# Performance work log

Hardware: AMD Instinct MI355X
Metric: run time of the kernel (lower is better)

## Reference

```python
import jax, jax.numpy as jnp
import numpy as np

EPS = 1e-5

def _ln(x, g, b):
    m = x.mean(-1, keepdims=True)
    v = ((x - m) ** 2).mean(-1, keepdims=True)
    return (x - m) * jax.lax.rsqrt(v + EPS) * g + b

def _tshift(x):
    # ZeroPad2d((0,0,1,-1)): xx[:, t] = x[:, t-1], xx[:, 0] = 0
    return jnp.concatenate([jnp.zeros_like(x[:, :1]), x[:, :-1]], axis=1)

def _wkv(time_decay, time_first, k, v):
    # Numerically-stable RWKV-4 WKV recurrence. k, v: (B, T, D)
    w = -jnp.exp(time_decay)  # (D,) negative decay
    u = time_first
    kT = jnp.swapaxes(k, 0, 1)  # (T, B, D)
    vT = jnp.swapaxes(v, 0, 1)
    a0 = jnp.zeros(kT.shape[1:], k.dtype)
    init = (a0, a0, jnp.full_like(a0, -1e30))  # a, b, p (running max exponent)
    def step(carry, kv_t):
        a, b, p = carry
        kt, vt = kv_t
        ww = u + kt
        q = jnp.maximum(p, ww)
        e1 = jnp.exp(p - q)
        e2 = jnp.exp(ww - q)
        y = (e1 * a + e2 * vt) / (e1 * b + e2)
        ww2 = p + w
        q2 = jnp.maximum(ww2, kt)
        e1b = jnp.exp(ww2 - q2)
        e2b = jnp.exp(kt - q2)
        return (e1b * a + e2b * vt, e1b * b + e2b, q2), y
    _, y = jax.lax.scan(step, init, (kT, vT))
    return jnp.swapaxes(y, 0, 1)

def setup_inputs() -> dict:
    key = jax.random.key(0)
    B, T, C, DA, DF = 8, 2048, 1024, 1024, 4096
    n_layer, layer_id = 12, 1
    ks = jax.random.split(key, 10)
    s = 0.02
    # faithful RWKV time-mixing inits
    r01 = layer_id / (n_layer - 1)
    r1a0 = 1.0 - layer_id / n_layer
    ddd = (np.arange(C) / C).astype(np.float32)
    decay_speed = (-5 + 8 * (np.arange(DA) / (DA - 1)) ** (0.7 + 1.3 * r01)).astype(np.float32)
    zigzag = (np.array([(i + 1) % 3 - 1 for i in range(DA)], dtype=np.float32)) * 0.5
    inp = {
        'x': jax.random.normal(ks[0], (B, T, C), jnp.float32),
        'ln1_g': jnp.ones((C,)), 'ln1_b': jnp.zeros((C,)),
        'ln2_g': jnp.ones((C,)), 'ln2_b': jnp.zeros((C,)),
        'tm_k': jnp.asarray(ddd ** r1a0),
        'tm_v': jnp.asarray(ddd ** r1a0 + 0.3 * r01),
        'tm_r': jnp.asarray(ddd ** (0.5 * r1a0)),
        'time_decay': jnp.asarray(decay_speed),
        'time_first': jnp.asarray(np.float32(np.log(0.3)) + zigzag),
        'Wk': jax.random.normal(ks[1], (DA, C), jnp.float32) * s,
        'Wv': jax.random.normal(ks[2], (DA, C), jnp.float32) * s,
        'Wr': jax.random.normal(ks[3], (DA, C), jnp.float32) * s,
        'Wo': jax.random.normal(ks[4], (C, DA), jnp.float32) * s,
        'fm_k': jnp.asarray(ddd ** r1a0),
        'fm_r': jnp.asarray(ddd ** r1a0),
        'Fk': jax.random.normal(ks[5], (DF, C), jnp.float32) * s,
        'Fr': jax.random.normal(ks[6], (C, C), jnp.float32) * s,
        'Fv': jax.random.normal(ks[7], (C, DF), jnp.float32) * s,
    }
    return inp

def reference(x, ln1_g, ln1_b, ln2_g, ln2_b, tm_k, tm_v, tm_r, time_decay, time_first,
              Wk, Wv, Wr, Wo, fm_k, fm_r, Fk, Fr, Fv):
    # --- TimeMix (RWKV attention) ---
    h = _ln(x, ln1_g, ln1_b)
    hh = _tshift(h)
    xk = h * tm_k + hh * (1 - tm_k)
    xv = h * tm_v + hh * (1 - tm_v)
    xr = h * tm_r + hh * (1 - tm_r)
    k = jnp.einsum('btc,dc->btd', xk, Wk)
    v = jnp.einsum('btc,dc->btd', xv, Wv)
    sr = jax.nn.sigmoid(jnp.einsum('btc,dc->btd', xr, Wr))
    rwkv = sr * _wkv(time_decay, time_first, k, v)
    x = x + jnp.einsum('btd,cd->btc', rwkv, Wo)
    # --- ChannelMix ---
    g = _ln(x, ln2_g, ln2_b)
    gg = _tshift(g)
    gk = g * fm_k + gg * (1 - fm_k)
    gr = g * fm_r + gg * (1 - fm_r)
    kf = jnp.square(jax.nn.relu(jnp.einsum('btc,fc->btf', gk, Fk)))
    kv = jnp.einsum('btf,cf->btc', kf, Fv)
    x = x + jax.nn.sigmoid(jnp.einsum('btc,dc->btd', gr, Fr)) * kv
    return x
```

## Files before the change

kernel.cpp:

```cpp
#include <hip/hip_runtime.h>
#include <stdint.h>

typedef __attribute__((ext_vector_type(4))) float f32x4;
typedef __attribute__((ext_vector_type(8))) __bf16 bfv8;

__device__ __forceinline__ ushort f2bf(float f) {
  union { float f; uint32_t u; } c; c.f = f;
  uint32_t u = c.u;
  uint32_t r = (u + 0x7fffu + ((u >> 16) & 1u)) >> 16;
  return (ushort)r;
}
__device__ __forceinline__ float bf2f(ushort h) {
  union { uint32_t u; float f; } c;
  c.u = ((uint32_t)h) << 16;
  return c.f;
}

__global__ void cvt_bf16(const float* __restrict__ src, ushort* __restrict__ dst, int n4) {
  int i = blockIdx.x * blockDim.x + threadIdx.x;
  if (i < n4) {
    float4 f = ((const float4*)src)[i];
    ushort4 o;
    o.x = f2bf(f.x); o.y = f2bf(f.y); o.z = f2bf(f.z); o.w = f2bf(f.w);
    ((ushort4*)dst)[i] = o;
  }
}

template <int NOUT, bool BI>
__global__ __launch_bounds__(256)
void ln_mix(const void* __restrict__ xin, const float* __restrict__ gam,
            const float* __restrict__ bet, const float* __restrict__ mk,
            const float* __restrict__ mv, const float* __restrict__ mr,
            ushort* __restrict__ ok, ushort* __restrict__ ov,
            ushort* __restrict__ orr, int T, int C) {
  const int row = blockIdx.x;
  const int t = row % T;
  const int tid = threadIdx.x;
  float4 c4, p4 = make_float4(0.f, 0.f, 0.f, 0.f);
  if constexpr (BI) {
    const ushort4* xc = (const ushort4*)((const ushort*)xin + (size_t)row * C);
    ushort4 u = xc[tid];
    c4 = make_float4(bf2f(u.x), bf2f(u.y), bf2f(u.z), bf2f(u.w));
    if (t > 0) {
      ushort4 up = xc[tid - (C >> 2)];
      p4 = make_float4(bf2f(up.x), bf2f(up.y), bf2f(up.z), bf2f(up.w));
    }
  } else {
    const float4* xc = (const float4*)((const float*)xin + (size_t)row * C);
    c4 = xc[tid];
    if (t > 0) p4 = xc[tid - (C >> 2)];
  }

  float s = c4.x + c4.y + c4.z + c4.w;
  float ss = c4.x * c4.x + c4.y * c4.y + c4.z * c4.z + c4.w * c4.w;
  float s2 = p4.x + p4.y + p4.z + p4.w;
  float ss2 = p4.x * p4.x + p4.y * p4.y + p4.z * p4.z + p4.w * p4.w;
#pragma unroll
  for (int off = 32; off > 0; off >>= 1) {
    s += __shfl_down(s, off);
    ss += __shfl_down(ss, off);
    s2 += __shfl_down(s2, off);
    ss2 += __shfl_down(ss2, off);
  }
  __shared__ float red[4][4];
  const int wid = tid >> 6, lane = tid & 63;
  if (lane == 0) { red[wid][0] = s; red[wid][1] = ss; red[wid][2] = s2; red[wid][3] = ss2; }
  __syncthreads();
  s = red[0][0] + red[1][0] + red[2][0] + red[3][0];
  ss = red[0][1] + red[1][1] + red[2][1] + red[3][1];
  s2 = red[0][2] + red[1][2] + red[2][2] + red[3][2];
  ss2 = red[0][3] + red[1][3] + red[2][3] + red[3][3];

  const float invC = 1.0f / (float)C;
  float m1 = s * invC, v1 = ss * invC - m1 * m1;
  float rs1 = rsqrtf(v1 + 1e-5f);
  float m2 = s2 * invC, v2 = ss2 * invC - m2 * m2;
  float rs2 = rsqrtf(v2 + 1e-5f);

  const float* c4p = (const float*)&c4;
  const float* p4p = (const float*)&p4;
  ushort4 vk, vv, vr;
#pragma unroll
  for (int j = 0; j < 4; j++) {
    int col = tid * 4 + j;
    float gg = gam[col], be = bet[col];
    float hc = (c4p[j] - m1) * rs1 * gg + be;
    float hp = (t > 0) ? ((p4p[j] - m2) * rs2 * gg + be) : 0.0f;
    float fk = mk[col];
    ((ushort*)&vk)[j] = f2bf(hc * fk + hp * (1.0f - fk));
    if constexpr (NOUT == 3) {
      float fv = mv[col];
      ((ushort*)&vv)[j] = f2bf(hc * fv + hp * (1.0f - fv));
    }
    float fr = mr[col];
    ((ushort*)&vr)[j] = f2bf(hc * fr + hp * (1.0f - fr));
  }
  size_t o = (size_t)row * (C >> 2) + tid;
  ((ushort4*)ok)[o] = vk;
  if constexpr (NOUT == 3) ((ushort4*)ov)[o] = vv;
  ((ushort4*)orr)[o] = vr;
}

template <int MODE>
__global__ __launch_bounds__(256, 2)
void gemm_bt(const ushort* __restrict__ A, const ushort* __restrict__ W,
             void* __restrict__ outp, const void* __restrict__ res,
             const ushort* __restrict__ mul, int N, int K) {
  __shared__ ushort lA[2][4096];
  __shared__ ushort lB[2][4096];
  const int tid = threadIdx.x;
  const int wave = tid >> 6, lane = tid & 63;

  const int nwg = gridDim.x * gridDim.y;
  const int bid = blockIdx.y * gridDim.x + blockIdx.x;
  const int swz = (bid & 7) * (nwg >> 3) + (bid >> 3);
  const int rowBase = (swz / gridDim.x) * 128;
  const int colBase = (swz % gridDim.x) * 128;

  const int wr = wave >> 1, wc = wave & 1;
  const int lr = lane & 15, lk = lane >> 4;

  f32x4 acc[4][4];
#pragma unroll
  for (int m = 0; m < 4; m++)
#pragma unroll
    for (int n = 0; n < 4; n++) acc[m][n] = (f32x4){0.f, 0.f, 0.f, 0.f};

  const int c0 = wave * 128 + lane;
  const int r0 = c0 >> 2, q0 = (c0 & 3) * 8;
  const int c1 = c0 + 64;
  const int r1 = c1 >> 2, q1 = (c1 & 3) * 8;

  auto stage = [&](int buf, int kt) {
    const ushort* gA0 = A + (size_t)(rowBase + r0) * K + kt + q0;
    const ushort* gA1 = A + (size_t)(rowBase + r1) * K + kt + q1;
    const ushort* gB0 = W + (size_t)(colBase + r0) * K + kt + q0;
    const ushort* gB1 = W + (size_t)(colBase + r1) * K + kt + q1;
    ushort* dA = &lA[buf][wave * 1024];
    ushort* dB = &lB[buf][wave * 1024];
    __builtin_amdgcn_global_load_lds(
        (const __attribute__((address_space(1))) void*)gA0,
        (__attribute__((address_space(3))) void*)dA, 16, 0, 0);
    __builtin_amdgcn_global_load_lds(
        (const __attribute__((address_space(1))) void*)gA1,
        (__attribute__((address_space(3))) void*)(dA + 512), 16, 0, 0);
    __builtin_amdgcn_global_load_lds(
        (const __attribute__((address_space(1))) void*)gB0,
        (__attribute__((address_space(3))) void*)dB, 16, 0, 0);
    __builtin_amdgcn_global_load_lds(
        (const __attribute__((address_space(1))) void*)gB1,
        (__attribute__((address_space(3))) void*)(dB + 512), 16, 0, 0);
  };

  auto compute = [&](int buf) {
    bfv8 af[4], bfr[4];
#pragma unroll
    for (int m = 0; m < 4; m++)
      af[m] = *(const bfv8*)(&lA[buf][(wr * 64 + m * 16 + lr) * 32 + lk * 8]);
#pragma unroll
    for (int n = 0; n < 4; n++)
      bfr[n] = *(const bfv8*)(&lB[buf][(wc * 64 + n * 16 + lr) * 32 + lk * 8]);
#pragma unroll
    for (int m = 0; m < 4; m++)
#pragma unroll
      for (int n = 0; n < 4; n++)
        acc[m][n] = __builtin_amdgcn_mfma_f32_16x16x32_bf16(af[m], bfr[n], acc[m][n], 0, 0, 0);
  };

  stage(0, 0);
  __syncthreads();
  int cur = 0;
  for (int kt = 0; kt + 32 < K; kt += 32) {
    stage(cur ^ 1, kt + 32);
    compute(cur);
    __syncthreads();
    cur ^= 1;
  }
  compute(cur);

#pragma unroll
  for (int m = 0; m < 4; m++) {
#pragma unroll
    for (int j = 0; j < 4; j++) {
      int row = rowBase + wr * 64 + m * 16 + lk * 4 + j;
#pragma unroll
      for (int n = 0; n < 4; n++) {
        int col = colBase + wc * 64 + n * 16 + lr;
        float v = acc[m][n][j];
        size_t idx = (size_t)row * N + col;
        if constexpr (MODE == 0) {
          ((ushort*)outp)[idx] = f2bf(v);
        } else if constexpr (MODE == 1) {
          ((ushort*)outp)[idx] = f2bf(1.0f / (1.0f + __expf(-v)));
        } else if constexpr (MODE == 2) {
          float r = fmaxf(v, 0.0f);
          ((ushort*)outp)[idx] = f2bf(r * r);
        } else if constexpr (MODE == 4) {
          ((float*)outp)[idx] = bf2f(((const ushort*)res)[idx]) + bf2f(mul[idx]) * v;
        } else {
          ((ushort*)outp)[idx] = f2bf(((const float*)res)[idx] + v);
        }
      }
    }
  }
}

#define WKV_NCH 32
#define WKV_L 64

__global__ __launch_bounds__(256)
void wkv_phase1(const ushort* __restrict__ k, const ushort* __restrict__ v,
                const float* __restrict__ td,
                float* __restrict__ sA, float* __restrict__ sB, float* __restrict__ sP,
                int T, int D) {
  int id = blockIdx.x * 256 + threadIdx.x;
  int d = id % D;
  int bc = id / D;
  int c = bc % WKV_NCH;
  int b = bc / WKV_NCH;
  float w = -__expf(td[d]);
  float a = 0.f, bb = 0.f, p = -1e30f;
  const size_t base = (size_t)b * T * D + (size_t)c * WKV_L * D + d;
#pragma unroll 4
  for (int t = 0; t < WKV_L; t++) {
    size_t idx = base + (size_t)t * D;
    float kt = bf2f(k[idx]), vt = bf2f(v[idx]);
    float ww2 = p + w;
    float q2 = fmaxf(ww2, kt);
    float e1b = __expf(ww2 - q2), e2b = __expf(kt - q2);
    a = e1b * a + e2b * vt;
    bb = e1b * bb + e2b;
    p = q2;
  }
  sA[id] = a; sB[id] = bb; sP[id] = p;
}

__global__ __launch_bounds__(256)
void wkv_combine(const float* __restrict__ td,
                 float* __restrict__ sA, float* __restrict__ sB, float* __restrict__ sP,
                 int D) {
  int id = blockIdx.x * 256 + threadIdx.x;
  int d = id % D;
  int b = id / D;
  float w = -__expf(td[d]);
  float Lw = (float)WKV_L * w;
  float a = 0.f, bb = 0.f, p = -1e30f;
  for (int c = 0; c < WKV_NCH; c++) {
    size_t idx = ((size_t)b * WKV_NCH + c) * D + d;
    float la = sA[idx], lb = sB[idx], lp = sP[idx];
    sA[idx] = a; sB[idx] = bb; sP[idx] = p;
    float pd = p + Lw;
    float q = fmaxf(pd, lp);
    float e1 = __expf(pd - q), e2 = __expf(lp - q);
    a = e1 * a + e2 * la;
    bb = e1 * bb + e2 * lb;
    p = q;
  }
}

__global__ __launch_bounds__(256)
void wkv_phase3(const ushort* __restrict__ k, const ushort* __restrict__ v,
                const ushort* __restrict__ sr, const float* __restrict__ td,
                const float* __restrict__ tf,
                const float* __restrict__ sA, const float* __restrict__ sB,
                const float* __restrict__ sP, ushort* __restrict__ out,
                int T, int D) {
  int id = blockIdx.x * 256 + threadIdx.x;
  int d = id % D;
  int bc = id / D;
  int c = bc % WKV_NCH;
  int b = bc / WKV_NCH;
  float w = -__expf(td[d]);
  float u = tf[d];
  float a = sA[id], bb = sB[id], p = sP[id];
  const size_t base = (size_t)b * T * D + (size_t)c * WKV_L * D + d;
#pragma unroll 2
  for (int t = 0; t < WKV_L; t++) {
    size_t idx = base + (size_t)t * D;
    float kt = bf2f(k[idx]), vt = bf2f(v[idx]);
    float ww = u + kt;
    float q = fmaxf(p, ww);
    float e1 = __expf(p - q), e2 = __expf(ww - q);
    float y = (e1 * a + e2 * vt) / (e1 * bb + e2);
    out[idx] = f2bf(bf2f(sr[idx]) * y);
    float ww2 = p + w;
    float q2 = fmaxf(ww2, kt);
    float e1b = __expf(ww2 - q2), e2b = __expf(kt - q2);
    a = e1b * a + e2b * vt;
    bb = e1b * bb + e2b;
    p = q2;
  }
}

extern "C" void kernel_launch(void* const* d_in, const int* in_sizes, int n_in,
                              void* d_out, int out_size, void* d_ws, size_t ws_size,
                              hipStream_t stream) {
  (void)in_sizes; (void)n_in; (void)out_size; (void)ws_size;
  const float* x    = (const float*)d_in[0];
  const float* ln1g = (const float*)d_in[1];
  const float* ln1b = (const float*)d_in[2];
  const float* ln2g = (const float*)d_in[3];
  const float* ln2b = (const float*)d_in[4];
  const float* tmk  = (const float*)d_in[5];
  const float* tmv  = (const float*)d_in[6];
  const float* tmr  = (const float*)d_in[7];
  const float* td   = (const float*)d_in[8];
  const float* tf   = (const float*)d_in[9];
  const float* Wk   = (const float*)d_in[10];
  const float* Wv   = (const float*)d_in[11];
  const float* Wr   = (const float*)d_in[12];
  const float* Wo   = (const float*)d_in[13];
  const float* fmk  = (const float*)d_in[14];
  const float* fmr  = (const float*)d_in[15];
  const float* Fk   = (const float*)d_in[16];
  const float* Fr   = (const float*)d_in[17];
  const float* Fv   = (const float*)d_in[18];

  const int B = 8, T = 2048, C = 1024, DA = 1024, DF = 4096;
  const int M = B * T;
  const int MH = M / 2;

  char* ws = (char*)d_ws;
  const size_t MiB = 1ull << 20;
  ushort* wkb = (ushort*)(ws + 0 * MiB);
  ushort* wvb = (ushort*)(ws + 2 * MiB);
  ushort* wrb = (ushort*)(ws + 4 * MiB);
  ushort* wob = (ushort*)(ws + 6 * MiB);
  ushort* fkb = (ushort*)(ws + 8 * MiB);
  ushort* frb = (ushort*)(ws + 16 * MiB);
  ushort* fvb = (ushort*)(ws + 18 * MiB);
  ushort* bufA = (ushort*)(ws + 26 * MiB);
  ushort* bufB = (ushort*)(ws + 58 * MiB);
  ushort* bufC = (ushort*)(ws + 90 * MiB);
  ushort* bufD = (ushort*)(ws + 122 * MiB);
  ushort* bufE = (ushort*)(ws + 154 * MiB);
  float*  sAa  = (float*)(ws + 186 * MiB);
  float*  sBb  = (float*)(ws + 187 * MiB);
  float*  sPp  = (float*)(ws + 188 * MiB);

  cvt_bf16<<<(DA * C / 4 + 255) / 256, 256, 0, stream>>>(Wk, wkb, DA * C / 4);
  cvt_bf16<<<(DA * C / 4 + 255) / 256, 256, 0, stream>>>(Wv, wvb, DA * C / 4);
  cvt_bf16<<<(DA * C / 4 + 255) / 256, 256, 0, stream>>>(Wr, wrb, DA * C / 4);
  cvt_bf16<<<(C * DA / 4 + 255) / 256, 256, 0, stream>>>(Wo, wob, C * DA / 4);
  cvt_bf16<<<(DF * C / 4 + 255) / 256, 256, 0, stream>>>(Fk, fkb, DF * C / 4);
  cvt_bf16<<<(C * C / 4 + 255) / 256, 256, 0, stream>>>(Fr, frb, C * C / 4);
  cvt_bf16<<<(C * DF / 4 + 255) / 256, 256, 0, stream>>>(Fv, fvb, C * DF / 4);

  ushort* xk = bufA; ushort* xv = bufB; ushort* xr = bufC;
  ln_mix<3, false><<<M, 256, 0, stream>>>(x, ln1g, ln1b, tmk, tmv, tmr, xk, xv, xr, T, C);

  ushort* kb = bufD; ushort* vb = bufA; ushort* srb = bufB; ushort* rwkv = bufC;
  dim3 gA(DA / 128, M / 128);
  gemm_bt<0><<<gA, 256, 0, stream>>>(xk, wkb, kb, nullptr, nullptr, DA, C);
  gemm_bt<0><<<gA, 256, 0, stream>>>(xv, wvb, vb, nullptr, nullptr, DA, C);
  gemm_bt<1><<<gA, 256, 0, stream>>>(xr, wrb, srb, nullptr, nullptr, DA, C);

  wkv_phase1<<<(B * WKV_NCH * DA) / 256, 256, 0, stream>>>(kb, vb, td, sAa, sBb, sPp, T, DA);
  wkv_combine<<<(B * DA) / 256, 256, 0, stream>>>(td, sAa, sBb, sPp, DA);
  wkv_phase3<<<(B * WKV_NCH * DA) / 256, 256, 0, stream>>>(kb, vb, srb, td, tf, sAa, sBb, sPp, rwkv, T, DA);

  ushort* xmidb = bufA;
  gemm_bt<5><<<dim3(C / 128, M / 128), 256, 0, stream>>>(rwkv, wob, xmidb, x, nullptr, C, DA);

  ushort* gk = bufB; ushort* gr = bufD; ushort* sig = bufE;
  ln_mix<2, true><<<M, 256, 0, stream>>>(xmidb, ln2g, ln2b, fmk, nullptr, fmr, gk, nullptr, gr, T, C);

  gemm_bt<1><<<dim3(C / 128, M / 128), 256, 0, stream>>>(gr, frb, sig, nullptr, nullptr, C, C);

  ushort* kf = bufC;
  for (int h = 0; h < 2; h++) {
    const ushort* gkh = gk + (size_t)h * MH * C;
    gemm_bt<2><<<dim3(DF / 128, MH / 128), 256, 0, stream>>>(gkh, fkb, kf, nullptr, nullptr, DF, C);
    gemm_bt<4><<<dim3(C / 128, MH / 128), 256, 0, stream>>>(
        kf, fvb, (float*)d_out + (size_t)h * MH * C,
        xmidb + (size_t)h * MH * C, sig + (size_t)h * MH * C, C, DF);
  }
}
```

Measured before the change: 878.0 us.

## Replace 128x128 GEMM with 256x256 triple-buffered swizzled-LDS GEMM and unsplit FFN

Replaces the 128x128 double-buffered GEMM with a 512-thread 256x256 tile kernel. It uses a three-stage LDS ring with XOR-swizzled layout, split staging interleaved with two MFMA halves, explicit vmcnt waits and s_setprio. The larger tile is meant to raise arithmetic intensity and cut LDS bank conflicts, while the deeper pipeline hides global loads. When the workspace is large enough, the FFN runs as one pass instead of two halves. In exchange, register pressure rises with 128 accumulators per thread, and there are fewer workgroups (e.g. 256 for the N=1024 GEMMs) to fill the CUs.

Result: faster. 773.5 us (-11.9%).

```diff
diff --git a/kernel.cpp b/kernel.cpp
--- a/kernel.cpp
+++ b/kernel.cpp
@@ -102,87 +102,104 @@
 }
 
 template <int MODE>
-__global__ __launch_bounds__(256, 2)
-void gemm_bt(const ushort* __restrict__ A, const ushort* __restrict__ W,
+__global__ __launch_bounds__(512, 2)
+void gemm256(const ushort* __restrict__ A, const ushort* __restrict__ W,
              void* __restrict__ outp, const void* __restrict__ res,
              const ushort* __restrict__ mul, int N, int K) {
-  __shared__ ushort lA[2][4096];
-  __shared__ ushort lB[2][4096];
+  __shared__ ushort lds[3 * 16384];
   const int tid = threadIdx.x;
   const int wave = tid >> 6, lane = tid & 63;
-
   const int nwg = gridDim.x * gridDim.y;
   const int bid = blockIdx.y * gridDim.x + blockIdx.x;
-  const int swz = (bid & 7) * (nwg >> 3) + (bid >> 3);
-  const int rowBase = (swz / gridDim.x) * 128;
-  const int colBase = (swz % gridDim.x) * 128;
-
-  const int wr = wave >> 1, wc = wave & 1;
+  const int swzb = (bid & 7) * (nwg >> 3) + (bid >> 3);
+  const int rowBase = (swzb / gridDim.x) * 256;
+  const int colBase = (swzb % gridDim.x) * 256;
+  const int wr = wave >> 2, wc = wave & 3;
   const int lr = lane & 15, lk = lane >> 4;
 
-  f32x4 acc[4][4];
-#pragma unroll
-  for (int m = 0; m < 4; m++)
+  f32x4 acc[8][4];
+#pragma unroll
+  for (int m = 0; m < 8; m++)
 #pragma unroll
     for (int n = 0; n < 4; n++) acc[m][n] = (f32x4){0.f, 0.f, 0.f, 0.f};
 
-  const int c0 = wave * 128 + lane;
-  const int r0 = c0 >> 2, q0 = (c0 & 3) * 8;
-  const int c1 = c0 + 64;
-  const int r1 = c1 >> 2, q1 = (c1 & 3) * 8;
-
-  auto stage = [&](int buf, int kt) {
-    const ushort* gA0 = A + (size_t)(rowBase + r0) * K + kt + q0;
-    const ushort* gA1 = A + (size_t)(rowBase + r1) * K + kt + q1;
-    const ushort* gB0 = W + (size_t)(colBase + r0) * K + kt + q0;
-    const ushort* gB1 = W + (size_t)(colBase + r1) * K + kt + q1;
-    ushort* dA = &lA[buf][wave * 1024];
-    ushort* dB = &lB[buf][wave * 1024];
+  const int NT = K >> 5;
+
+  auto stage = [&](int s, int kt, int j) {
+    int c = (wave * 2 + j) * 64 + lane;
+    int r = c >> 2;
+    int cb = ((c & 3) << 4) ^ (((r >> 1) & 3) << 4);
+    const ushort* srcA = A + (size_t)(rowBase + r) * K + kt + (cb >> 1);
+    const ushort* srcB = W + (size_t)(colBase + r) * K + kt + (cb >> 1);
+    ushort* dA = &lds[s * 16384 + (wave * 2 + j) * 512];
     __builtin_amdgcn_global_load_lds(
-        (const __attribute__((address_space(1))) void*)gA0,
+        (const __attribute__((address_space(1))) void*)srcA,
         (__attribute__((address_space(3))) void*)dA, 16, 0, 0);
     __builtin_amdgcn_global_load_lds(
-        (const __attribute__((address_space(1))) void*)gA1,
-        (__attribute__((address_space(3))) void*)(dA + 512), 16, 0, 0);
-    __builtin_amdgcn_global_load_lds(
-        (const __attribute__((address_space(1))) void*)gB0,
-        (__attribute__((address_space(3))) void*)dB, 16, 0, 0);
-    __builtin_amdgcn_global_load_lds(
-        (const __attribute__((address_space(1))) void*)gB1,
-        (__attribute__((address_space(3))) void*)(dB + 512), 16, 0, 0);
+        (const __attribute__((address_space(1))) void*)srcB,
+        (__attribute__((address_space(3))) void*)(dA + 8192), 16, 0, 0);
   };
 
-  auto compute = [&](int buf) {
+  stage(0, 0, 0); stage(0, 0, 1);
+  stage(1, 32, 0); stage(1, 32, 1);
+  asm volatile("s_waitcnt vmcnt(4)" ::: "memory");
+  __builtin_amdgcn_s_barrier();
+
+  int cs = 0;
+  for (int t = 0; t < NT; ++t) {
+    const int ns = (cs + 2 >= 3) ? cs - 1 : cs + 2;
+    const ushort* As = &lds[cs * 16384];
+    const ushort* Bs = As + 8192;
+    const bool doStage = (t + 2) < NT;
+    const int kt2 = (t + 2) << 5;
+
     bfv8 af[4], bfr[4];
-#pragma unroll
-    for (int m = 0; m < 4; m++)
-      af[m] = *(const bfv8*)(&lA[buf][(wr * 64 + m * 16 + lr) * 32 + lk * 8]);
-#pragma unroll
-    for (int n = 0; n < 4; n++)
-      bfr[n] = *(const bfv8*)(&lB[buf][(wc * 64 + n * 16 + lr) * 32 + lk * 8]);
+    if (doStage) stage(ns, kt2, 0);
+#pragma unroll
+    for (int m = 0; m < 4; m++) {
+      int row = wr * 128 + m * 16 + lr;
+      af[m] = *(const bfv8*)(As + row * 32 + ((lk * 8) ^ (((row >> 1) & 3) << 3)));
+    }
+#pragma unroll
+    for (int n = 0; n < 4; n++) {
+      int row = wc * 64 + n * 16 + lr;
+      bfr[n] = *(const bfv8*)(Bs + row * 32 + ((lk * 8) ^ (((row >> 1) & 3) << 3)));
+    }
+    __builtin_amdgcn_s_barrier();
+    __builtin_amdgcn_s_setprio(1);
 #pragma unroll
     for (int m = 0; m < 4; m++)
 #pragma unroll
       for (int n = 0; n < 4; n++)
         acc[m][n] = __builtin_amdgcn_mfma_f32_16x16x32_bf16(af[m], bfr[n], acc[m][n], 0, 0, 0);
-  };
-
-  stage(0, 0);
-  __syncthreads();
-  int cur = 0;
-  for (int kt = 0; kt + 32 < K; kt += 32) {
-    stage(cur ^ 1, kt + 32);
-    compute(cur);
-    __syncthreads();
-    cur ^= 1;
-  }
-  compute(cur);
-
-#pragma unroll
-  for (int m = 0; m < 4; m++) {
+    __builtin_amdgcn_s_setprio(0);
+    __builtin_amdgcn_s_barrier();
+
+    if (doStage) stage(ns, kt2, 1);
+#pragma unroll
+    for (int m = 0; m < 4; m++) {
+      int row = wr * 128 + (m + 4) * 16 + lr;
+      af[m] = *(const bfv8*)(As + row * 32 + ((lk * 8) ^ (((row >> 1) & 3) << 3)));
+    }
+    __builtin_amdgcn_s_barrier();
+    __builtin_amdgcn_s_setprio(1);
+#pragma unroll
+    for (int m = 0; m < 4; m++)
+#pragma unroll
+      for (int n = 0; n < 4; n++)
+        acc[m + 4][n] = __builtin_amdgcn_mfma_f32_16x16x32_bf16(af[m], bfr[n], acc[m + 4][n], 0, 0, 0);
+    __builtin_amdgcn_s_setprio(0);
+    if (doStage) { asm volatile("s_waitcnt vmcnt(4)" ::: "memory"); }
+    else         { asm volatile("s_waitcnt vmcnt(0)" ::: "memory"); }
+    __builtin_amdgcn_s_barrier();
+    cs = (cs == 2) ? 0 : cs + 1;
+  }
+
+#pragma unroll
+  for (int m = 0; m < 8; m++) {
 #pragma unroll
     for (int j = 0; j < 4; j++) {
-      int row = rowBase + wr * 64 + m * 16 + lk * 4 + j;
+      int row = rowBase + wr * 128 + m * 16 + lk * 4 + j;
 #pragma unroll
       for (int n = 0; n < 4; n++) {
         int col = colBase + wc * 64 + n * 16 + lr;
@@ -295,7 +312,7 @@
 extern "C" void kernel_launch(void* const* d_in, const int* in_sizes, int n_in,
                               void* d_out, int out_size, void* d_ws, size_t ws_size,
                               hipStream_t stream) {
-  (void)in_sizes; (void)n_in; (void)out_size; (void)ws_size;
+  (void)in_sizes; (void)n_in; (void)out_size;
   const float* x    = (const float*)d_in[0];
   const float* ln1g = (const float*)d_in[1];
   const float* ln1b = (const float*)d_in[2];
@@ -320,6 +337,8 @@
   const int M = B * T;
   const int MH = M / 2;
 
+  const bool fullffn = ws_size >= (251ull << 20);
+
   char* ws = (char*)d_ws;
   const size_t MiB = 1ull << 20;
   ushort* wkb = (ushort*)(ws + 0 * MiB);
@@ -333,10 +352,18 @@
   ushort* bufB = (ushort*)(ws + 58 * MiB);
   ushort* bufC = (ushort*)(ws + 90 * MiB);
   ushort* bufD = (ushort*)(ws + 122 * MiB);
-  ushort* bufE = (ushort*)(ws + 154 * MiB);
-  float*  sAa  = (float*)(ws + 186 * MiB);
-  float*  sBb  = (float*)(ws + 187 * MiB);
-  float*  sPp  = (float*)(ws + 188 * MiB);
+  float* sAa; float* sBb; float* sPp; ushort* sig;
+  if (fullffn) {
+    sAa = (float*)(ws + 154 * MiB);
+    sBb = (float*)(ws + 155 * MiB);
+    sPp = (float*)(ws + 156 * MiB);
+    sig = (ushort*)(ws + 218 * MiB);
+  } else {
+    sig = (ushort*)(ws + 154 * MiB);
+    sAa = (float*)(ws + 186 * MiB);
+    sBb = (float*)(ws + 187 * MiB);
+    sPp = (float*)(ws + 188 * MiB);
+  }
 
   cvt_bf16<<<(DA * C / 4 + 255) / 256, 256, 0, stream>>>(Wk, wkb, DA * C / 4);
   cvt_bf16<<<(DA * C / 4 + 255) / 256, 256, 0, stream>>>(Wv, wvb, DA * C / 4);
@@ -350,29 +377,34 @@
   ln_mix<3, false><<<M, 256, 0, stream>>>(x, ln1g, ln1b, tmk, tmv, tmr, xk, xv, xr, T, C);
 
   ushort* kb = bufD; ushort* vb = bufA; ushort* srb = bufB; ushort* rwkv = bufC;
-  dim3 gA(DA / 128, M / 128);
-  gemm_bt<0><<<gA, 256, 0, stream>>>(xk, wkb, kb, nullptr, nullptr, DA, C);
-  gemm_bt<0><<<gA, 256, 0, stream>>>(xv, wvb, vb, nullptr, nullptr, DA, C);
-  gemm_bt<1><<<gA, 256, 0, stream>>>(xr, wrb, srb, nullptr, nullptr, DA, C);
+  dim3 gQ(DA / 256, M / 256);
+  gemm256<0><<<gQ, 512, 0, stream>>>(xk, wkb, kb, nullptr, nullptr, DA, C);
+  gemm256<0><<<gQ, 512, 0, stream>>>(xv, wvb, vb, nullptr, nullptr, DA, C);
+  gemm256<1><<<gQ, 512, 0, stream>>>(xr, wrb, srb, nullptr, nullptr, DA, C);
 
   wkv_phase1<<<(B * WKV_NCH * DA) / 256, 256, 0, stream>>>(kb, vb, td, sAa, sBb, sPp, T, DA);
   wkv_combine<<<(B * DA) / 256, 256, 0, stream>>>(td, sAa, sBb, sPp, DA);
   wkv_phase3<<<(B * WKV_NCH * DA) / 256, 256, 0, stream>>>(kb, vb, srb, td, tf, sAa, sBb, sPp, rwkv, T, DA);
 
   ushort* xmidb = bufA;
-  gemm_bt<5><<<dim3(C / 128, M / 128), 256, 0, stream>>>(rwkv, wob, xmidb, x, nullptr, C, DA);
-
-  ushort* gk = bufB; ushort* gr = bufD; ushort* sig = bufE;
+  gemm256<5><<<dim3(C / 256, M / 256), 512, 0, stream>>>(rwkv, wob, xmidb, x, nullptr, C, DA);
+
+  ushort* gk = bufB; ushort* gr = bufD;
   ln_mix<2, true><<<M, 256, 0, stream>>>(xmidb, ln2g, ln2b, fmk, nullptr, fmr, gk, nullptr, gr, T, C);
 
-  gemm_bt<1><<<dim3(C / 128, M / 128), 256, 0, stream>>>(gr, frb, sig, nullptr, nullptr, C, C);
+  gemm256<1><<<dim3(C / 256, M / 256), 512, 0, stream>>>(gr, frb, sig, nullptr, nullptr, C, C);
 
   ushort* kf = bufC;
-  for (int h = 0; h < 2; h++) {
-    const ushort* gkh = gk + (size_t)h * MH * C;
-    gemm_bt<2><<<dim3(DF / 128, MH / 128), 256, 0, stream>>>(gkh, fkb, kf, nullptr, nullptr, DF, C);
-    gemm_bt<4><<<dim3(C / 128, MH / 128), 256, 0, stream>>>(
-        kf, fvb, (float*)d_out + (size_t)h * MH * C,
-        xmidb + (size_t)h * MH * C, sig + (size_t)h * MH * C, C, DF);
-  }
-}
+  if (fullffn) {
+    gemm256<2><<<dim3(DF / 256, M / 256), 512, 0, stream>>>(gk, fkb, kf, nullptr, nullptr, DF, C);
+    gemm256<4><<<dim3(C / 256, M / 256), 512, 0, stream>>>(kf, fvb, (float*)d_out, xmidb, sig, C, DF);
+  } else {
+    for (int h = 0; h < 2; h++) {
+      const ushort* gkh = gk + (size_t)h * MH * C;
+      gemm256<2><<<dim3(DF / 256, MH / 256), 512, 0, stream>>>(gkh, fkb, kf, nullptr, nullptr, DF, C);
+      gemm256<4><<<dim3(C / 256, MH / 256), 512, 0, stream>>>(
+          kf, fvb, (float*)d_out + (size_t)h * MH * C,
+          xmidb + (size_t)h * MH * C, sig + (size_t)h * MH * C, C, DF);
+    }
+  }
+}
```
